# Optimization experiments

Hardware: AMD Instinct MI355X
Metric: run time of the kernel (lower is better)

The kernel has to match this reference:

```python
import jax, jax.numpy as jnp
import numpy as np

B, L, D, H = 1, 4096, 1024, 16
HD = D // H  # head dim = 64
WINDOW = 15


def _rope(t, cos, sin):
    # t: [B,H,L,HD]; cos/sin: [1,1,L,HD//2]
    tr = t.reshape(*t.shape[:-1], HD // 2, 2)
    a, b = tr[..., 0], tr[..., 1]
    out_r = a * cos - b * sin
    out_i = a * sin + b * cos
    return jnp.stack([out_r, out_i], axis=-1).reshape(t.shape)


def _longformer_mask(L, window):
    i = jnp.arange(L)[:, None]
    j = jnp.arange(L)[None, :]
    causal = j <= i
    win = jnp.abs(i - j) <= window // 2
    glob = (j == 0) | (i == 0)
    return (causal & win) | glob  # [L,L] bool


def setup_inputs() -> dict:
    key = jax.random.key(0)
    kx, kq, kk, kv, ko = jax.random.split(key, 5)
    x = jax.random.normal(kx, (B, L, D), dtype=jnp.float32)
    scale = 0.02
    Wq = jax.random.normal(kq, (D, D), dtype=jnp.float32) * scale
    Wk = jax.random.normal(kk, (D, D), dtype=jnp.float32) * scale
    Wv = jax.random.normal(kv, (D, D), dtype=jnp.float32) * scale
    Wo = jax.random.normal(ko, (D, D), dtype=jnp.float32) * scale
    # real RoPE frequencies (complex freqs_cis split into cos/sin)
    inv_freq = 1.0 / (10000.0 ** (np.arange(0, HD, 2, dtype=np.float32) / HD))
    pos = np.arange(L, dtype=np.float32)
    ang = pos[:, None] * inv_freq[None, :]  # [L, HD//2]
    freqs_cos = jnp.asarray(np.cos(ang))[None]  # [1,L,HD//2]
    freqs_sin = jnp.asarray(np.sin(ang))[None]
    return {"x": x, "Wq": Wq, "Wk": Wk, "Wv": Wv, "Wo": Wo,
            "freqs_cos": freqs_cos, "freqs_sin": freqs_sin}


def reference(x, Wq, Wk, Wv, Wo, freqs_cos, freqs_sin):
    b, l, _ = x.shape
    # projections (nn.Linear: y = x @ W^T)
    Q = (x @ Wq.T).reshape(b, l, H, HD).transpose(0, 2, 1, 3)  # [B,H,L,HD]
    K = (x @ Wk.T).reshape(b, l, H, HD).transpose(0, 2, 1, 3)
    V = (x @ Wv.T).reshape(b, l, H, HD).transpose(0, 2, 1, 3)
    cos = freqs_cos[:, None, :l]  # [1,1,L,HD//2] (torch unsqueeze(1))
    sin = freqs_sin[:, None, :l]
    Q = _rope(Q, cos, sin)
    K = _rope(K, cos, sin)
    mask = _longformer_mask(l, WINDOW)  # [L,L]
    scores = jnp.einsum('bhqd,bhkd->bhqk', Q, K) / jnp.sqrt(jnp.float32(HD))
    scores = jnp.where(mask[None, None], scores, jnp.finfo(scores.dtype).min)
    attn = jax.nn.softmax(scores, axis=-1)
    out = jnp.einsum('bhqk,bhkd->bhqd', attn, V)  # [B,H,L,HD]
    out = out.transpose(0, 2, 1, 3).reshape(b, l, D)
    return out @ Wo.T
```

## Files before the change

kernel.cpp:

```cpp
#include <hip/hip_runtime.h>
#include <stdint.h>

#define SL 4096
#define DM 1024
#define NH 16
#define HDIM 64

typedef short short8 __attribute__((ext_vector_type(8)));
typedef float f32x4 __attribute__((ext_vector_type(4)));

__device__ __forceinline__ unsigned short f2bf(float f) {
  unsigned int u = __float_as_uint(f);
  u += 0x7FFF + ((u >> 16) & 1);
  return (unsigned short)(u >> 16);
}
__device__ __forceinline__ float bf2f(unsigned short u) {
  return __uint_as_float((unsigned int)u << 16);
}
__device__ __forceinline__ float bflo(unsigned int u) { return __uint_as_float(u << 16); }
__device__ __forceinline__ float bfhi(unsigned int u) { return __uint_as_float(u & 0xffff0000u); }

__device__ __forceinline__ void gload_lds16(const void* g, void* l) {
  __builtin_amdgcn_global_load_lds((const __attribute__((address_space(1))) void*)g,
                                   (__attribute__((address_space(3))) void*)l, 16, 0, 0);
}
#define SBAR()                                  \
  do {                                          \
    __builtin_amdgcn_sched_barrier(0);          \
    __builtin_amdgcn_s_barrier();               \
    __builtin_amdgcn_sched_barrier(0);          \
  } while (0)
#define LGKM0() asm volatile("s_waitcnt lgkmcnt(0)" ::: "memory")

__global__ void cast_all(const float* __restrict__ x,
                         const float* __restrict__ Wq, const float* __restrict__ Wk,
                         const float* __restrict__ Wv, const float* __restrict__ Wo,
                         unsigned short* __restrict__ xb,
                         unsigned short* __restrict__ w3b, unsigned short* __restrict__ wob) {
  int i = blockIdx.x * blockDim.x + threadIdx.x;
  const float* src;
  unsigned short* dst;
  int off;
  if (i < (1 << 20)) {
    src = x; dst = xb; off = i;
  } else {
    int wsel = i - (1 << 20);
    int seg = wsel >> 18;
    off = wsel & 262143;
    src = (seg == 0) ? Wq : (seg == 1) ? Wk : (seg == 2) ? Wv : Wo;
    dst = (seg < 3) ? (w3b + (size_t)seg * DM * DM) : wob;
  }
  float4 v = ((const float4*)src)[off];
  ushort4 o = make_ushort4(f2bf(v.x), f2bf(v.y), f2bf(v.z), f2bf(v.w));
  ((ushort4*)dst)[off] = o;
}

__global__ __launch_bounds__(512, 4)
void gemm1_rope(const unsigned short* __restrict__ A,
                const unsigned short* __restrict__ B,
                unsigned short* __restrict__ C,
                const float* __restrict__ fc, const float* __restrict__ fs) {
  constexpr int K = 1024, LDA = 1024, LDC = 3072, NT = K / 64;
  __shared__ __align__(16) unsigned short As[2][128 * 64];
  __shared__ __align__(16) unsigned short Bs[2][192 * 64];
  const int tid = threadIdx.x, w = tid >> 6, lane = tid & 63;
  const int wr = w >> 2, wc = w & 3;

  const int gx = gridDim.x;
  const int total = gx * gridDim.y;
  const int lin = blockIdx.y * gx + blockIdx.x;
  const int swz = (lin & 7) * (total >> 3) + (lin >> 3);
  const int brow = (swz / gx) * 128;
  const int bcol = (swz % gx) * 192;

  const unsigned short* gA[2];
  const unsigned short* gB[3];
#pragma unroll
  for (int l = 0; l < 2; ++l) {
    int idx = l * 512 + tid;
    int row_l = idx >> 3, c = idx & 7;
    int csrc = c ^ ((row_l >> 1) & 7);
    gA[l] = A + (size_t)(brow + row_l) * LDA + csrc * 8;
  }
#pragma unroll
  for (int l = 0; l < 3; ++l) {
    int idx = l * 512 + tid;
    int row_l = idx >> 3, c = idx & 7;
    int csrc = c ^ ((row_l >> 1) & 7);
    gB[l] = B + (size_t)(bcol + row_l) * LDA + csrc * 8;
  }

  auto STG_A = [&](int t) {
    const int buf = t & 1;
#pragma unroll
    for (int l = 0; l < 2; ++l)
      gload_lds16(gA[l] + t * 64, &As[buf][(l * 512 + w * 64) * 8]);
  };
  auto STG_B_all = [&](int t) {
    const int buf = t & 1;
#pragma unroll
    for (int l = 0; l < 3; ++l)
      gload_lds16(gB[l] + t * 64, &Bs[buf][(l * 512 + w * 64) * 8]);
  };

  const int lrow = lane & 15, h4 = lane >> 4;
  const int g3 = (lane >> 1) & 7;
  const int u2 = h4 ^ (g3 & 3);
  const int gv = g3 >> 2;
  const int co0 = ((((0 ^ gv) << 2) | u2)) * 8;
  const int co1 = ((((1 ^ gv) << 2) | u2)) * 8;

  f32x4 acc[4][3] = {};
  short8 a0[4], a1[4], b0[3], b1[3];

  STG_A(0); STG_B_all(0);
  STG_A(1); STG_B_all(1);
  asm volatile("s_waitcnt vmcnt(5)" ::: "memory");
  SBAR();

  for (int t = 0; t < NT; ++t) {
    const int buf = t & 1;
    const unsigned short* Ab = &As[buf][(wr * 64 + lrow) * 64];
    const unsigned short* Bb = &Bs[buf][(wc * 48 + lrow) * 64];
#pragma unroll
    for (int n = 0; n < 3; ++n) b0[n] = *(const short8*)&Bb[n * 16 * 64 + co0];
#pragma unroll
    for (int m = 0; m < 4; ++m) a0[m] = *(const short8*)&Ab[m * 16 * 64 + co0];
    SBAR();
    __builtin_amdgcn_s_setprio(1);
#pragma unroll
    for (int m = 0; m < 4; ++m)
#pragma unroll
      for (int n = 0; n < 3; ++n)
        acc[m][n] = __builtin_amdgcn_mfma_f32_16x16x32_bf16(a0[m], b0[n], acc[m][n], 0, 0, 0);
    __builtin_amdgcn_s_setprio(0);
#pragma unroll
    for (int n = 0; n < 3; ++n) b1[n] = *(const short8*)&Bb[n * 16 * 64 + co1];
#pragma unroll
    for (int m = 0; m < 4; ++m) a1[m] = *(const short8*)&Ab[m * 16 * 64 + co1];
    LGKM0();
    SBAR();
    __builtin_amdgcn_s_setprio(1);
#pragma unroll
    for (int m = 0; m < 4; ++m)
      acc[m][0] = __builtin_amdgcn_mfma_f32_16x16x32_bf16(a1[m], b1[0], acc[m][0], 0, 0, 0);
    __builtin_amdgcn_s_setprio(0);
    if (t + 2 < NT) { STG_A(t + 2); STG_B_all(t + 2); }
    if (t >= NT - 2) {
      asm volatile("s_waitcnt vmcnt(0)" ::: "memory");
    } else {
      asm volatile("s_waitcnt vmcnt(5)" ::: "memory");
    }
    SBAR();
    __builtin_amdgcn_s_setprio(1);
#pragma unroll
    for (int m = 0; m < 4; ++m) {
      acc[m][1] = __builtin_amdgcn_mfma_f32_16x16x32_bf16(a1[m], b1[1], acc[m][1], 0, 0, 0);
      acc[m][2] = __builtin_amdgcn_mfma_f32_16x16x32_bf16(a1[m], b1[2], acc[m][2], 0, 0, 0);
    }
    __builtin_amdgcn_s_setprio(0);
  }

  const int er = (lane >> 4) * 4;
  const int ec = lane & 15;
#pragma unroll
  for (int n = 0; n < 3; ++n) {
    if (bcol + wc * 48 + n * 16 < 2048) {
      const int p = ((wc * 48 + n * 16 + ec) & 63) >> 1;
#pragma unroll
      for (int m = 0; m < 4; ++m) {
#pragma unroll
        for (int r = 0; r < 4; ++r) {
          const int row = brow + wr * 64 + m * 16 + er + r;
          float v = acc[m][n][r];
          float pv = __shfl_xor(v, 1);
          float cs = fc[row * 32 + p], sn = fs[row * 32 + p];
          acc[m][n][r] = (lane & 1) ? (pv * sn + v * cs) : (v * cs - pv * sn);
        }
      }
    }
  }
#pragma unroll
  for (int m = 0; m < 4; ++m)
#pragma unroll
    for (int n = 0; n < 3; ++n) {
      unsigned short* cp = C + (size_t)(brow + wr * 64 + m * 16 + er) * LDC +
                           (bcol + wc * 48 + n * 16 + ec);
#pragma unroll
      for (int r = 0; r < 4; ++r) cp[(size_t)r * LDC] = f2bf(acc[m][n][r]);
    }
}

__global__ __launch_bounds__(512)
void gemm2_bk128(const unsigned short* __restrict__ A,
                 const unsigned short* __restrict__ B,
                 float* __restrict__ C) {
  constexpr int K = 1024, LDA = 1024, LDC = 1024, NT = K / 128;
  __shared__ __align__(16) unsigned short As2[2][2][128 * 64];
  __shared__ __align__(16) unsigned short Bs2[2][2][128 * 64];
  const int tid = threadIdx.x, w = tid >> 6, lane = tid & 63;
  const int wr = w >> 2, wc = w & 3;

  const int gx = gridDim.x;
  const int total = gx * gridDim.y;
  const int lin = blockIdx.y * gx + blockIdx.x;
  const int swz = (lin & 7) * (total >> 3) + (lin >> 3);
  const int brow = (swz / gx) * 128;
  const int bcol = (swz % gx) * 128;

  const unsigned short* gA[2];
  const unsigned short* gB[2];
#pragma unroll
  for (int l = 0; l < 2; ++l) {
    int idx = l * 512 + tid;
    int row_l = idx >> 3, c = idx & 7;
    int csrc = c ^ ((row_l >> 1) & 7);
    gA[l] = A + (size_t)(brow + row_l) * LDA + csrc * 8;
    gB[l] = B + (size_t)(bcol + row_l) * LDA + csrc * 8;
  }

  auto STG_A = [&](int t, int h) {
    const int buf = t & 1;
#pragma unroll
    for (int l = 0; l < 2; ++l)
      gload_lds16(gA[l] + t * 128 + h * 64, &As2[buf][h][(l * 512 + w * 64) * 8]);
  };
  auto STG_B = [&](int t, int h) {
    const int buf = t & 1;
#pragma unroll
    for (int l = 0; l < 2; ++l)
      gload_lds16(gB[l] + t * 128 + h * 64, &Bs2[buf][h][(l * 512 + w * 64) * 8]);
  };

  const int lrow = lane & 15, h4 = lane >> 4;
  const int g3 = (lane >> 1) & 7;
  const int u2 = h4 ^ (g3 & 3);
  const int gv = g3 >> 2;
  const int co0 = ((((0 ^ gv) << 2) | u2)) * 8;
  const int co1 = ((((1 ^ gv) << 2) | u2)) * 8;

  f32x4 acc[4][2] = {};
  short8 a0[4], a1[4], a2[4], a3[4], b0[2], b1[2], b2[2], b3[2];

  STG_A(0, 0); STG_A(0, 1); STG_B(0, 0); STG_B(0, 1);
  STG_A(1, 0); STG_A(1, 1); STG_B(1, 0); STG_B(1, 1);
  asm volatile("s_waitcnt vmcnt(8)" ::: "memory");
  SBAR();

  for (int t = 0; t < NT; ++t) {
    const int buf = t & 1;
    const unsigned short* Ab0 = &As2[buf][0][(wr * 64 + lrow) * 64];
    const unsigned short* Ab1 = &As2[buf][1][(wr * 64 + lrow) * 64];
    const unsigned short* Bb0 = &Bs2[buf][0][(wc * 32 + lrow) * 64];
    const unsigned short* Bb1 = &Bs2[buf][1][(wc * 32 + lrow) * 64];
#pragma unroll
    for (int n = 0; n < 2; ++n) { b0[n] = *(const short8*)&Bb0[n * 16 * 64 + co0];
                                  b1[n] = *(const short8*)&Bb0[n * 16 * 64 + co1]; }
#pragma unroll
    for (int m = 0; m < 4; ++m) { a0[m] = *(const short8*)&Ab0[m * 16 * 64 + co0];
                                  a1[m] = *(const short8*)&Ab0[m * 16 * 64 + co1]; }
    SBAR();
    __builtin_amdgcn_s_setprio(1);
#pragma unroll
    for (int m = 0; m < 4; ++m)
#pragma unroll
      for (int n = 0; n < 2; ++n)
        acc[m][n] = __builtin_amdgcn_mfma_f32_16x16x32_bf16(a0[m], b0[n], acc[m][n], 0, 0, 0);
    __builtin_amdgcn_s_setprio(0);
#pragma unroll
    for (int n = 0; n < 2; ++n) { b2[n] = *(const short8*)&Bb1[n * 16 * 64 + co0];
                                  b3[n] = *(const short8*)&Bb1[n * 16 * 64 + co1]; }
#pragma unroll
    for (int m = 0; m < 4; ++m) { a2[m] = *(const short8*)&Ab1[m * 16 * 64 + co0];
                                  a3[m] = *(const short8*)&Ab1[m * 16 * 64 + co1]; }
    LGKM0();
    SBAR();
    __builtin_amdgcn_s_setprio(1);
#pragma unroll
    for (int m = 0; m < 4; ++m)
#pragma unroll
      for (int n = 0; n < 2; ++n)
        acc[m][n] = __builtin_amdgcn_mfma_f32_16x16x32_bf16(a1[m], b1[n], acc[m][n], 0, 0, 0);
    __builtin_amdgcn_s_setprio(0);
    if (t + 2 < NT) { STG_A(t + 2, 0); STG_B(t + 2, 0); STG_A(t + 2, 1); STG_B(t + 2, 1); }
    if (t >= NT - 2) {
      asm volatile("s_waitcnt vmcnt(0)" ::: "memory");
    } else {
      asm volatile("s_waitcnt vmcnt(8)" ::: "memory");
    }
    SBAR();
    __builtin_amdgcn_s_setprio(1);
#pragma unroll
    for (int m = 0; m < 4; ++m)
#pragma unroll
      for (int n = 0; n < 2; ++n) {
        acc[m][n] = __builtin_amdgcn_mfma_f32_16x16x32_bf16(a2[m], b2[n], acc[m][n], 0, 0, 0);
        acc[m][n] = __builtin_amdgcn_mfma_f32_16x16x32_bf16(a3[m], b3[n], acc[m][n], 0, 0, 0);
      }
    __builtin_amdgcn_s_setprio(0);
  }

  const int er = (lane >> 4) * 4;
  const int ec = lane & 15;
#pragma unroll
  for (int m = 0; m < 4; ++m)
#pragma unroll
    for (int n = 0; n < 2; ++n) {
      float* cp = C + (size_t)(brow + wr * 64 + m * 16 + er) * LDC +
                  (bcol + wc * 32 + n * 16 + ec);
#pragma unroll
      for (int r = 0; r < 4; ++r)
        __builtin_nontemporal_store(acc[m][n][r], cp + (size_t)r * LDC);
    }
}

__global__ __launch_bounds__(256)
void attn_fused(const unsigned short* __restrict__ qkv, unsigned short* __restrict__ atb,
                float* __restrict__ prt) {
  const int wid = threadIdx.x >> 6;
  const int lane = threadIdx.x & 63;
  if (blockIdx.x >= 1024) {
    const int u = (blockIdx.x - 1024) * 4 + wid;
    const int p = u & 127, h = u >> 7;
    const float q = bf2f(qkv[h * 64 + lane]);
    float m = -1e30f, s = 0.f, o = 0.f;
    const int j0 = p * 32;
    for (int jj = 0; jj < 32; ++jj) {
      const int j = j0 + jj;
      float kv = bf2f(qkv[(size_t)j * 3072 + 1024 + h * 64 + lane]);
      float pr = q * kv;
#pragma unroll
      for (int off = 32; off; off >>= 1) pr += __shfl_xor(pr, off);
      pr *= 0.125f;
      float mn = fmaxf(m, pr);
      float c = __expf(m - mn);
      float e = __expf(pr - mn);
      float v = bf2f(qkv[(size_t)j * 3072 + 2048 + h * 64 + lane]);
      s = s * c + e;
      o = o * c + e * v;
      m = mn;
    }
    float* dst = prt + ((size_t)h * 128 + p) * 72;
    if (lane == 0) { dst[0] = m; dst[1] = s; }
    dst[2 + lane] = o;
    return;
  }

  const int i = blockIdx.x * 4 + wid + 1;
  if (i >= SL) return;
  const unsigned short* rowQ = qkv + (size_t)i * 3072 + lane * 16;

  float q[16];
  {
    uint4 a = *(const uint4*)rowQ;
    uint4 b = *(const uint4*)(rowQ + 8);
    unsigned int uu[8] = {a.x, a.y, a.z, a.w, b.x, b.y, b.z, b.w};
#pragma unroll
    for (int c = 0; c < 8; ++c) { q[2 * c] = bflo(uu[c]); q[2 * c + 1] = bfhi(uu[c]); }
  }

  float sc[9];
#pragma unroll
  for (int t = 0; t < 9; ++t) {
    int j = (t == 0) ? 0 : (i - 8 + t);
    bool valid = (t == 0) || (j >= 1);
    int jc = valid ? j : 0;
    const unsigned short* pk = qkv + (size_t)jc * 3072 + 1024 + lane * 16;
    uint4 a = *(const uint4*)pk;
    uint4 b = *(const uint4*)(pk + 8);
    unsigned int uu[8] = {a.x, a.y, a.z, a.w, b.x, b.y, b.z, b.w};
    float pr = 0.f;
#pragma unroll
    for (int c = 0; c < 8; ++c) pr += bflo(uu[c]) * q[2 * c] + bfhi(uu[c]) * q[2 * c + 1];
    pr += __shfl_xor(pr, 1);
    pr += __shfl_xor(pr, 2);
    sc[t] = valid ? pr * 0.125f : -1e30f;
  }

  float mx = sc[0];
#pragma unroll
  for (int t = 1; t < 9; ++t) mx = fmaxf(mx, sc[t]);
  float s = 0.f;
#pragma unroll
  for (int t = 0; t < 9; ++t) { float e = __expf(sc[t] - mx); sc[t] = e; s += e; }
  const float inv = 1.0f / s;

  float o[16] = {};
#pragma unroll
  for (int t = 0; t < 9; ++t) {
    int j = (t == 0) ? 0 : (i - 8 + t);
    bool valid = (t == 0) || (j >= 1);
    int jc = valid ? j : 0;
    const unsigned short* pv = qkv + (size_t)jc * 3072 + 2048 + lane * 16;
    uint4 a = *(const uint4*)pv;
    uint4 b = *(const uint4*)(pv + 8);
    unsigned int uu[8] = {a.x, a.y, a.z, a.w, b.x, b.y, b.z, b.w};
#pragma unroll
    for (int c = 0; c < 8; ++c) {
      o[2 * c]     += sc[t] * bflo(uu[c]);
      o[2 * c + 1] += sc[t] * bfhi(uu[c]);
    }
  }

  unsigned int wv[8];
#pragma unroll
  for (int c = 0; c < 8; ++c)
    wv[c] = (unsigned int)f2bf(o[2 * c] * inv) | ((unsigned int)f2bf(o[2 * c + 1] * inv) << 16);
  unsigned short* po = atb + (size_t)i * 1024 + lane * 16;
  uint4 s0; s0.x = wv[0]; s0.y = wv[1]; s0.z = wv[2]; s0.w = wv[3];
  uint4 s1; s1.x = wv[4]; s1.y = wv[5]; s1.z = wv[6]; s1.w = wv[7];
  *(uint4*)po = s0;
  *(uint4*)(po + 8) = s1;
}

__global__ __launch_bounds__(64)
void attn_row0_combine(const float* __restrict__ prt, unsigned short* __restrict__ atb) {
  const int h = blockIdx.x;
  const int lane = threadIdx.x;
  const float* base = prt + (size_t)h * 128 * 72;
  __shared__ float cbuf[128];
  float m0 = base[lane * 72];
  float m1 = base[(lane + 64) * 72];
  float M = fmaxf(m0, m1);
#pragma unroll
  for (int off = 32; off; off >>= 1) M = fmaxf(M, __shfl_xor(M, off));
  float c0 = __expf(m0 - M), c1 = __expf(m1 - M);
  float ls = base[lane * 72 + 1] * c0 + base[(lane + 64) * 72 + 1] * c1;
#pragma unroll
  for (int off = 32; off; off >>= 1) ls += __shfl_xor(ls, off);
  cbuf[lane] = c0;
  cbuf[lane + 64] = c1;
  __syncthreads();
  float o = 0.f;
#pragma unroll 8
  for (int p = 0; p < 128; ++p) o += cbuf[p] * base[p * 72 + 2 + lane];
  atb[h * 64 + lane] = f2bf(o / ls);
}

extern "C" void kernel_launch(void* const* d_in, const int* in_sizes, int n_in,
                              void* d_out, int out_size, void* d_ws, size_t ws_size,
                              hipStream_t stream) {
  const float* x  = (const float*)d_in[0];
  const float* Wq = (const float*)d_in[1];
  const float* Wk = (const float*)d_in[2];
  const float* Wv = (const float*)d_in[3];
  const float* Wo = (const float*)d_in[4];
  const float* fc = (const float*)d_in[5];
  const float* fs = (const float*)d_in[6];
  float* out = (float*)d_out;

  char* ws = (char*)d_ws;
  unsigned short* xb   = (unsigned short*)(ws);
  unsigned short* w3b  = (unsigned short*)(ws + ((size_t)8 << 20));
  unsigned short* wob  = (unsigned short*)(ws + ((size_t)14 << 20));
  unsigned short* qkvb = (unsigned short*)(ws + ((size_t)16 << 20));
  unsigned short* atb  = (unsigned short*)(ws + ((size_t)40 << 20));
  float*          prt  = (float*)(ws + ((size_t)48 << 20));

  cast_all<<<(2 * (1 << 20)) / 256, 256, 0, stream>>>(x, Wq, Wk, Wv, Wo, xb, w3b, wob);

  dim3 g1(3072 / 192, SL / 128);
  gemm1_rope<<<g1, 512, 0, stream>>>(xb, w3b, qkvb, fc, fs);

  attn_fused<<<1536, 256, 0, stream>>>(qkvb, atb, prt);
  attn_row0_combine<<<NH, 64, 0, stream>>>(prt, atb);

  dim3 g2(DM / 128, SL / 128);
  gemm2_bk128<<<g2, 512, 0, stream>>>(atb, wob, out);
}
```

Baseline: 85.15 us.

## Triple-buffer LDS in QKV GEMM and use single barrier per K-step

```diff
diff --git a/kernel.cpp b/kernel.cpp
--- a/kernel.cpp
+++ b/kernel.cpp
@@ -55,14 +55,14 @@
   ((ushort4*)dst)[off] = o;
 }
 
-__global__ __launch_bounds__(512, 4)
+__global__ __launch_bounds__(512, 2)
 void gemm1_rope(const unsigned short* __restrict__ A,
                 const unsigned short* __restrict__ B,
                 unsigned short* __restrict__ C,
                 const float* __restrict__ fc, const float* __restrict__ fs) {
   constexpr int K = 1024, LDA = 1024, LDC = 3072, NT = K / 64;
-  __shared__ __align__(16) unsigned short As[2][128 * 64];
-  __shared__ __align__(16) unsigned short Bs[2][192 * 64];
+  __shared__ __align__(16) unsigned short As[3][128 * 64];
+  __shared__ __align__(16) unsigned short Bs[3][192 * 64];
   const int tid = threadIdx.x, w = tid >> 6, lane = tid & 63;
   const int wr = w >> 2, wc = w & 3;
 
@@ -90,14 +90,11 @@
     gB[l] = B + (size_t)(bcol + row_l) * LDA + csrc * 8;
   }
 
-  auto STG_A = [&](int t) {
-    const int buf = t & 1;
+  auto STG = [&](int t) {
+    const int buf = t % 3;
 #pragma unroll
     for (int l = 0; l < 2; ++l)
       gload_lds16(gA[l] + t * 64, &As[buf][(l * 512 + w * 64) * 8]);
-  };
-  auto STG_B_all = [&](int t) {
-    const int buf = t & 1;
 #pragma unroll
     for (int l = 0; l < 3; ++l)
       gload_lds16(gB[l] + t * 64, &Bs[buf][(l * 512 + w * 64) * 8]);
@@ -113,51 +110,39 @@
   f32x4 acc[4][3] = {};
   short8 a0[4], a1[4], b0[3], b1[3];
 
-  STG_A(0); STG_B_all(0);
-  STG_A(1); STG_B_all(1);
+  STG(0); STG(1);
   asm volatile("s_waitcnt vmcnt(5)" ::: "memory");
   SBAR();
 
   for (int t = 0; t < NT; ++t) {
-    const int buf = t & 1;
+    const int buf = t % 3;
     const unsigned short* Ab = &As[buf][(wr * 64 + lrow) * 64];
     const unsigned short* Bb = &Bs[buf][(wc * 48 + lrow) * 64];
 #pragma unroll
-    for (int n = 0; n < 3; ++n) b0[n] = *(const short8*)&Bb[n * 16 * 64 + co0];
-#pragma unroll
-    for (int m = 0; m < 4; ++m) a0[m] = *(const short8*)&Ab[m * 16 * 64 + co0];
-    SBAR();
-    __builtin_amdgcn_s_setprio(1);
-#pragma unroll
-    for (int m = 0; m < 4; ++m)
-#pragma unroll
-      for (int n = 0; n < 3; ++n)
-        acc[m][n] = __builtin_amdgcn_mfma_f32_16x16x32_bf16(a0[m], b0[n], acc[m][n], 0, 0, 0);
-    __builtin_amdgcn_s_setprio(0);
-#pragma unroll
-    for (int n = 0; n < 3; ++n) b1[n] = *(const short8*)&Bb[n * 16 * 64 + co1];
-#pragma unroll
-    for (int m = 0; m < 4; ++m) a1[m] = *(const short8*)&Ab[m * 16 * 64 + co1];
-    LGKM0();
-    SBAR();
-    __builtin_amdgcn_s_setprio(1);
-#pragma unroll
-    for (int m = 0; m < 4; ++m)
-      acc[m][0] = __builtin_amdgcn_mfma_f32_16x16x32_bf16(a1[m], b1[0], acc[m][0], 0, 0, 0);
-    __builtin_amdgcn_s_setprio(0);
-    if (t + 2 < NT) { STG_A(t + 2); STG_B_all(t + 2); }
+    for (int n = 0; n < 3; ++n) { b0[n] = *(const short8*)&Bb[n * 16 * 64 + co0];
+                                  b1[n] = *(const short8*)&Bb[n * 16 * 64 + co1]; }
+#pragma unroll
+    for (int m = 0; m < 4; ++m) { a0[m] = *(const short8*)&Ab[m * 16 * 64 + co0];
+                                  a1[m] = *(const short8*)&Ab[m * 16 * 64 + co1]; }
+    if (t + 2 < NT) STG(t + 2);
     if (t >= NT - 2) {
       asm volatile("s_waitcnt vmcnt(0)" ::: "memory");
     } else {
       asm volatile("s_waitcnt vmcnt(5)" ::: "memory");
     }
+    LGKM0();
     SBAR();
     __builtin_amdgcn_s_setprio(1);
 #pragma unroll
-    for (int m = 0; m < 4; ++m) {
-      acc[m][1] = __builtin_amdgcn_mfma_f32_16x16x32_bf16(a1[m], b1[1], acc[m][1], 0, 0, 0);
-      acc[m][2] = __builtin_amdgcn_mfma_f32_16x16x32_bf16(a1[m], b1[2], acc[m][2], 0, 0, 0);
-    }
+    for (int m = 0; m < 4; ++m)
+#pragma unroll
+      for (int n = 0; n < 3; ++n)
+        acc[m][n] = __builtin_amdgcn_mfma_f32_16x16x32_bf16(a0[m], b0[n], acc[m][n], 0, 0, 0);
+#pragma unroll
+    for (int m = 0; m < 4; ++m)
+#pragma unroll
+      for (int n = 0; n < 3; ++n)
+        acc[m][n] = __builtin_amdgcn_mfma_f32_16x16x32_bf16(a1[m], b1[n], acc[m][n], 0, 0, 0);
     __builtin_amdgcn_s_setprio(0);
   }
 
```

Result: slower. 89.85 us (+5.5%).
